# Kernel tuning notes

Measured on AMD Instinct MI355X. Metric: run time of the kernel, lower is better.

## Reference

```python
import jax, jax.numpy as jnp
import numpy as np


def setup_inputs() -> dict:
    key = jax.random.key(0)
    k1, k2, k3 = jax.random.split(key, 3)
    B, C_in, H, W = 32, 128, 56, 56
    C_out, ksz = 256, 3
    x = jax.random.normal(k1, (B, C_in, H, W), dtype=jnp.float32)
    weight = jax.random.normal(k2, (C_out, C_in, ksz, ksz), dtype=jnp.float32) * 0.05
    bias = jax.random.normal(k3, (C_out,), dtype=jnp.float32)
    return {"x": x, "weight": weight, "bias": bias}


PADDING = 1
GROUPS = 1


def reference(x, weight, bias):
    # Same math as the manual pad+unfold+einsum: a standard stride-1 grouped
    # conv2d with symmetric zero padding. Expressed as implicit-GEMM conv.
    out = jax.lax.conv_general_dilated(
        x, weight,
        window_strides=(1, 1),
        padding=[(PADDING, PADDING), (PADDING, PADDING)],
        dimension_numbers=("NCHW", "OIHW", "NCHW"),
        feature_group_count=GROUPS,
    )
    out = out + bias[None, :, None, None]
    return out
```

## Files before the change

### kernel.cpp

```cpp
#include <hip/hip_runtime.h>
#include <stdint.h>

#define BATCH 32
#define CIN   128
#define HH    56
#define WW    56
#define COUT  256
#define HP    58
#define WP    58

typedef __attribute__((ext_vector_type(8))) short short8;
typedef __attribute__((ext_vector_type(4))) float floatx4;

#define GLOAD_LDS16(gptr, lptr)                                          \
  __builtin_amdgcn_global_load_lds(                                      \
      (const __attribute__((address_space(1))) void*)(gptr),             \
      (__attribute__((address_space(3))) void*)(lptr), 16, 0, 0)

__device__ __forceinline__ unsigned short f32_to_bf16(float f) {
  unsigned int u = __float_as_uint(f);
  u = u + 0x7fffu + ((u >> 16) & 1u);
  return (unsigned short)(u >> 16);
}
__device__ __forceinline__ unsigned int pack2(float a, float b) {
  return (unsigned int)f32_to_bf16(a) | ((unsigned int)f32_to_bf16(b) << 16);
}


__global__ void pad_transpose_kernel(const float* __restrict__ x,
                                     unsigned short* __restrict__ xpt) {
  const int blk = blockIdx.x;
  const int b = blk / HP;
  const int i = blk - b * HP;
  const int t = threadIdx.x;
  unsigned short* dst = xpt + (size_t)blk * (WP * CIN);

  if (i == 0 || i == HP - 1) {
    const uint4 z = {0, 0, 0, 0};
    for (int idx = t; idx < 928; idx += 256)
      *(uint4*)(dst + (size_t)idx * 8) = z;
    return;
  }

  __shared__ float tile[CIN * 59];
  tile[(t >> 1) * 59 + (t & 1) * 57] = 0.0f;
  {
    const int ci = t >> 1;
    const int seg = t & 1;
    const float* row =
        x + (((size_t)b * CIN + ci) * HH + (i - 1)) * WW + seg * 28;
    float* trow = tile + ci * 59 + 1 + seg * 28;
#pragma unroll
    for (int q = 0; q < 7; ++q) {
      const float4 v = *(const float4*)(row + q * 4);
      trow[q * 4 + 0] = v.x;
      trow[q * 4 + 1] = v.y;
      trow[q * 4 + 2] = v.z;
      trow[q * 4 + 3] = v.w;
    }
  }
  __syncthreads();
  for (int idx = t; idx < 928; idx += 256) {
    const int j = idx >> 4;
    const int ci0 = (idx & 15) * 8;
    uint4 pk;
    pk.x = pack2(tile[(ci0 + 0) * 59 + j], tile[(ci0 + 1) * 59 + j]);
    pk.y = pack2(tile[(ci0 + 2) * 59 + j], tile[(ci0 + 3) * 59 + j]);
    pk.z = pack2(tile[(ci0 + 4) * 59 + j], tile[(ci0 + 5) * 59 + j]);
    pk.w = pack2(tile[(ci0 + 6) * 59 + j], tile[(ci0 + 7) * 59 + j]);
    *(uint4*)(dst + (size_t)idx * 8) = pk;
  }
}

__global__ void weight_transpose_kernel(const float* __restrict__ wsrc,
                                        unsigned short* __restrict__ wt) {
  const int o8 = blockIdx.x * 256 + threadIdx.x;
  const int r = o8 >> 12;
  const int rem = o8 & 4095;
  const int co = rem >> 4;
  const int ci0 = (rem & 15) * 8;
  const float* s = wsrc + ((size_t)co * CIN + ci0) * 9 + r;
  uint4 pk;
  pk.x = pack2(s[0 * 9], s[1 * 9]);
  pk.y = pack2(s[2 * 9], s[3 * 9]);
  pk.z = pack2(s[4 * 9], s[5 * 9]);
  pk.w = pack2(s[6 * 9], s[7 * 9]);
  *(uint4*)(wt + (size_t)o8 * 8) = pk;
}

__global__ __launch_bounds__(256) void conv_gemm_kernel(
    const unsigned short* __restrict__ xpt,
    const unsigned short* __restrict__ wt,
    const float* __restrict__ bias,
    float* __restrict__ out) {
  __shared__ __align__(16) uint32_t smem[8192];
  short* const S = (short*)smem;
  short* const As0 = S;
  short* const As1 = S + 4096;
  short* const Bs0 = S + 8192;
  short* const Bs1 = S + 12288;
  float* const ep = (float*)smem;

  const int g = blockIdx.x;
  const int xcd = g & 7;
  const int jj = g >> 3;
  const int nt = jj & 1;
  const int mt = (jj >> 1) * 8 + xcd;
  const int b = mt / 28;
  const int h0 = (mt - b * 28) * 2;
  const int co0 = nt * 128;

  const int t = threadIdx.x;
  const int lane = t & 63;
  const int wv = t >> 6;
  const int mw = wv & 1;
  const int nw = wv >> 1;
  const int laneM = lane & 15;
  const int laneKg = lane >> 4;
  const int xk = (laneKg ^ (laneM & 3)) * 8;
  const int rowreg = laneKg * 4;

  const unsigned short* ag[2];
  const unsigned short* bg[2];
  short* al[2];
  short* bl[2];
#pragma unroll
  for (int c = 0; c < 2; ++c) {
    const int u = c * 256 + t;
    const int mm = u >> 2;
    const int j8 = (((u & 3) ^ (mm & 3)) * 8);
    const int hp0 = h0 + (mm >> 6);
    const int wc0 = mm & 63;
    ag[c] = xpt + ((size_t)((b * HP + hp0) * WP + wc0)) * CIN + j8;
    bg[c] = wt + (size_t)(co0 + mm) * CIN + j8;
    al[c] = As0 + (size_t)(c * 256 + wv * 64) * 8;
    bl[c] = Bs0 + (size_t)(c * 256 + wv * 64) * 8;
  }

  floatx4 acc[4][4] = {};

  for (int r = 0; r < 9; ++r) {
    const int dh = (r * 11) >> 5;
    const int dw = r - dh * 3;
    const int aoff = (dh * WP + dw) * CIN;
    const int boff = r * (COUT * CIN);
#pragma unroll
    for (int kt = 0; kt < 2; ++kt) {
      const int ci0 = kt * 64;
      GLOAD_LDS16(ag[0] + aoff + ci0, al[0]);
      GLOAD_LDS16(ag[1] + aoff + ci0, al[1]);
      GLOAD_LDS16(ag[0] + aoff + ci0 + 32, al[0] + 4096);
      GLOAD_LDS16(ag[1] + aoff + ci0 + 32, al[1] + 4096);
      GLOAD_LDS16(bg[0] + boff + ci0, bl[0]);
      GLOAD_LDS16(bg[1] + boff + ci0, bl[1]);
      GLOAD_LDS16(bg[0] + boff + ci0 + 32, bl[0] + 4096);
      GLOAD_LDS16(bg[1] + boff + ci0 + 32, bl[1] + 4096);
      __syncthreads();

#pragma unroll
      for (int half = 0; half < 2; ++half) {
        const short* Ah = half ? As1 : As0;
        const short* Bh = half ? Bs1 : Bs0;
        short8 af[4], bfr[4];
#pragma unroll
        for (int mi = 0; mi < 4; ++mi)
          af[mi] = *(const short8*)&Ah[(mw * 64 + mi * 16 + laneM) * 32 + xk];
#pragma unroll
        for (int ni = 0; ni < 4; ++ni)
          bfr[ni] = *(const short8*)&Bh[(nw * 64 + ni * 16 + laneM) * 32 + xk];
#pragma unroll
        for (int mi = 0; mi < 4; ++mi)
#pragma unroll
          for (int ni = 0; ni < 4; ++ni)
            acc[mi][ni] = __builtin_amdgcn_mfma_f32_16x16x32_bf16(
                af[mi], bfr[ni], acc[mi][ni], 0, 0, 0);
      }
      __syncthreads();
    }
  }

  for (int ni = 0; ni < 4; ++ni) {
    __syncthreads();
#pragma unroll
    for (int mi = 0; mi < 4; ++mi)
      *(float4*)&ep[(nw * 16 + laneM) * 132 + mw * 64 + mi * 16 + rowreg] =
          *(float4*)&acc[mi][ni];
    __syncthreads();
#pragma unroll
    for (int rr = 0; rr < 16; ++rr) {
      const int rowid = wv * 16 + rr;
      const int cg = rowid >> 1;
      const int hh = rowid & 1;
      const int co = co0 + (cg >> 4) * 64 + ni * 16 + (cg & 15);
      const float bv = bias[co];
      if (lane < WW) {
        out[(((size_t)b * COUT + co) * HH + h0 + hh) * WW + lane] =
            ep[cg * 132 + hh * 64 + lane] + bv;
      }
    }
  }
}

__global__ void naive_conv_kernel(const float* __restrict__ x,
                                  const float* __restrict__ wgt,
                                  const float* __restrict__ bias,
                                  float* __restrict__ out, long n) {
  long idx = (long)blockIdx.x * 256 + threadIdx.x;
  if (idx >= n) return;
  int w = (int)(idx % WW);
  long q = idx / WW;
  int h = (int)(q % HH);
  q /= HH;
  int co = (int)(q % COUT);
  int b = (int)(q / COUT);
  float s = bias[co];
  for (int ci = 0; ci < CIN; ++ci) {
    const float* xp = x + (((size_t)b * CIN + ci) * HH) * WW;
    const float* wp = wgt + ((size_t)co * CIN + ci) * 9;
    for (int dh = 0; dh < 3; ++dh) {
      int hh = h + dh - 1;
      if (hh < 0 || hh >= HH) continue;
      for (int dw = 0; dw < 3; ++dw) {
        int ww2 = w + dw - 1;
        if (ww2 < 0 || ww2 >= WW) continue;
        s += xp[hh * WW + ww2] * wp[dh * 3 + dw];
      }
    }
  }
  out[idx] = s;
}

extern "C" void kernel_launch(void* const* d_in, const int* in_sizes, int n_in,
                              void* d_out, int out_size, void* d_ws,
                              size_t ws_size, hipStream_t stream) {
  const float* x = (const float*)d_in[0];
  const float* wgt = (const float*)d_in[1];
  const float* bias = (const float*)d_in[2];
  float* out = (float*)d_out;

  const size_t XPT = (size_t)BATCH * HP * WP * CIN;
  const size_t SLACK = 1024;
  const size_t WT = (size_t)9 * COUT * CIN;
  const size_t need = (XPT + SLACK + WT) * sizeof(unsigned short);

  if (ws_size >= need) {
    unsigned short* xpt = (unsigned short*)d_ws;
    unsigned short* wtp = xpt + XPT + SLACK;
    hipLaunchKernelGGL(pad_transpose_kernel, dim3(BATCH * HP), dim3(256), 0,
                       stream, x, xpt);
    hipLaunchKernelGGL(weight_transpose_kernel, dim3(144), dim3(256), 0,
                       stream, wgt, wtp);
    hipLaunchKernelGGL(conv_gemm_kernel, dim3(896 * 2), dim3(256), 0, stream,
                       xpt, wtp, bias, out);
  } else {
    long n = (long)out_size;
    hipLaunchKernelGGL(naive_conv_kernel, dim3((unsigned)((n + 255) / 256)),
                       dim3(256), 0, stream, x, wgt, bias, out, n);
  }
}
```

Baseline: 217.6 us.

## Software-pipeline conv GEMM K loop with 4-stage LDS ring and prefetch depth two

Replaces the load-sync-compute-sync loop with a 36-step K loop over 32-wide slices held in a four-slot LDS ring. Each step issues global-to-LDS loads two slices ahead and waits on vmcnt, so there is one barrier per step instead of two and memory latency overlaps the MFMA work. It also changes the LDS swizzle to XOR two bit-groups of the row index, aiming to cut bank conflicts, and raises MFMA priority with s_setprio. LDS use doubles to 64KB per block and launch bounds now request two blocks per CU; the ring's correctness depends on the hand-written vmcnt counts matching the number of loads in flight.

```diff
diff --git a/kernel.cpp b/kernel.cpp
--- a/kernel.cpp
+++ b/kernel.cpp
@@ -88,17 +88,13 @@
   *(uint4*)(wt + (size_t)o8 * 8) = pk;
 }
 
-__global__ __launch_bounds__(256) void conv_gemm_kernel(
+__global__ __launch_bounds__(256, 2) void conv_gemm_kernel(
     const unsigned short* __restrict__ xpt,
     const unsigned short* __restrict__ wt,
     const float* __restrict__ bias,
     float* __restrict__ out) {
-  __shared__ __align__(16) uint32_t smem[8192];
+  __shared__ __align__(16) uint32_t smem[16384];
   short* const S = (short*)smem;
-  short* const As0 = S;
-  short* const As1 = S + 4096;
-  short* const Bs0 = S + 8192;
-  short* const Bs1 = S + 12288;
   float* const ep = (float*)smem;
 
   const int g = blockIdx.x;
@@ -117,66 +113,71 @@
   const int nw = wv >> 1;
   const int laneM = lane & 15;
   const int laneKg = lane >> 4;
-  const int xk = (laneKg ^ (laneM & 3)) * 8;
+  const int sw = (laneM & 3) ^ ((laneM >> 2) & 3);
+  const int xk = (laneKg ^ sw) * 8;
   const int rowreg = laneKg * 4;
 
   const unsigned short* ag[2];
   const unsigned short* bg[2];
-  short* al[2];
-  short* bl[2];
 #pragma unroll
   for (int c = 0; c < 2; ++c) {
     const int u = c * 256 + t;
     const int mm = u >> 2;
-    const int j8 = (((u & 3) ^ (mm & 3)) * 8);
+    const int smm = (mm & 3) ^ ((mm >> 2) & 3);
+    const int j8 = (((u & 3) ^ smm) * 8);
     const int hp0 = h0 + (mm >> 6);
     const int wc0 = mm & 63;
     ag[c] = xpt + ((size_t)((b * HP + hp0) * WP + wc0)) * CIN + j8;
     bg[c] = wt + (size_t)(co0 + mm) * CIN + j8;
-    al[c] = As0 + (size_t)(c * 256 + wv * 64) * 8;
-    bl[c] = Bs0 + (size_t)(c * 256 + wv * 64) * 8;
-  }
+  }
+  const int dA = wv * 512;
 
   floatx4 acc[4][4] = {};
 
-  for (int r = 0; r < 9; ++r) {
+  auto stageK = [&](int kk) {
+    const int r = kk >> 2;
     const int dh = (r * 11) >> 5;
     const int dw = r - dh * 3;
-    const int aoff = (dh * WP + dw) * CIN;
-    const int boff = r * (COUT * CIN);
-#pragma unroll
-    for (int kt = 0; kt < 2; ++kt) {
-      const int ci0 = kt * 64;
-      GLOAD_LDS16(ag[0] + aoff + ci0, al[0]);
-      GLOAD_LDS16(ag[1] + aoff + ci0, al[1]);
-      GLOAD_LDS16(ag[0] + aoff + ci0 + 32, al[0] + 4096);
-      GLOAD_LDS16(ag[1] + aoff + ci0 + 32, al[1] + 4096);
-      GLOAD_LDS16(bg[0] + boff + ci0, bl[0]);
-      GLOAD_LDS16(bg[1] + boff + ci0, bl[1]);
-      GLOAD_LDS16(bg[0] + boff + ci0 + 32, bl[0] + 4096);
-      GLOAD_LDS16(bg[1] + boff + ci0 + 32, bl[1] + 4096);
-      __syncthreads();
-
-#pragma unroll
-      for (int half = 0; half < 2; ++half) {
-        const short* Ah = half ? As1 : As0;
-        const short* Bh = half ? Bs1 : Bs0;
-        short8 af[4], bfr[4];
-#pragma unroll
-        for (int mi = 0; mi < 4; ++mi)
-          af[mi] = *(const short8*)&Ah[(mw * 64 + mi * 16 + laneM) * 32 + xk];
-#pragma unroll
-        for (int ni = 0; ni < 4; ++ni)
-          bfr[ni] = *(const short8*)&Bh[(nw * 64 + ni * 16 + laneM) * 32 + xk];
-#pragma unroll
-        for (int mi = 0; mi < 4; ++mi)
-#pragma unroll
-          for (int ni = 0; ni < 4; ++ni)
-            acc[mi][ni] = __builtin_amdgcn_mfma_f32_16x16x32_bf16(
-                af[mi], bfr[ni], acc[mi][ni], 0, 0, 0);
-      }
-      __syncthreads();
-    }
+    const int aoff = (dh * WP + dw) * CIN + (kk & 3) * 32;
+    const int boff = r * (COUT * CIN) + (kk & 3) * 32;
+    short* const base = S + (kk & 3) * 8192;
+    GLOAD_LDS16(ag[0] + aoff, base + dA);
+    GLOAD_LDS16(ag[1] + aoff, base + 2048 + dA);
+    GLOAD_LDS16(bg[0] + boff, base + 4096 + dA);
+    GLOAD_LDS16(bg[1] + boff, base + 4096 + 2048 + dA);
+  };
+
+  stageK(0);
+  stageK(1);
+  asm volatile("s_waitcnt vmcnt(4)" ::: "memory");
+  __builtin_amdgcn_s_barrier();
+  __builtin_amdgcn_sched_barrier(0);
+
+  for (int kk = 0; kk < 36; ++kk) {
+    const short* Ab = S + (kk & 3) * 8192;
+    const short* Bb = Ab + 4096;
+    short8 af[4], bfr[4];
+#pragma unroll
+    for (int mi = 0; mi < 4; ++mi)
+      af[mi] = *(const short8*)&Ab[(mw * 64 + mi * 16 + laneM) * 32 + xk];
+#pragma unroll
+    for (int ni = 0; ni < 4; ++ni)
+      bfr[ni] = *(const short8*)&Bb[(nw * 64 + ni * 16 + laneM) * 32 + xk];
+    if (kk < 34) stageK(kk + 2);
+    __builtin_amdgcn_s_setprio(1);
+#pragma unroll
+    for (int mi = 0; mi < 4; ++mi)
+#pragma unroll
+      for (int ni = 0; ni < 4; ++ni)
+        acc[mi][ni] = __builtin_amdgcn_mfma_f32_16x16x32_bf16(
+            af[mi], bfr[ni], acc[mi][ni], 0, 0, 0);
+    __builtin_amdgcn_s_setprio(0);
+    if (kk < 34)
+      asm volatile("s_waitcnt vmcnt(4)" ::: "memory");
+    else
+      asm volatile("s_waitcnt vmcnt(0)" ::: "memory");
+    __builtin_amdgcn_s_barrier();
+    __builtin_amdgcn_sched_barrier(0);
   }
 
   for (int ni = 0; ni < 4; ++ni) {
```

After: 220.6 us. Within noise of the previous version (+1.4%).
